# Kernel optimization log

Hardware: AMD Instinct MI355X
Metric: run time of the kernel (lower is better)

The kernel has to match this reference:

```python
import jax, jax.numpy as jnp
import numpy as np

N = 20000      # nodes
E = 256000     # edges
ESM = 1280     # esm_dim
H = 4          # heads
C = 256        # hidden_dim (per-head out)
HC = H * C     # 1024, concat width


def setup_inputs() -> dict:
    key = jax.random.key(0)
    ks = jax.random.split(key, 12)
    s = 0.02
    x = jax.random.normal(ks[0], (N, ESM), jnp.float32)
    edge_index = jax.random.randint(ks[1], (2, E), 0, N, dtype=jnp.int32)
    edge_weights = jax.random.uniform(ks[2], (E,), jnp.float32)
    # GATv2Conv params (PyG): lin_l (src, bias), lin_r (dst, no bias), lin_edge (no bias), att, out bias
    Wl = jax.random.normal(ks[3], (ESM, HC), jnp.float32) * s
    bl = jnp.zeros((HC,), jnp.float32)
    Wr = jax.random.normal(ks[4], (ESM, HC), jnp.float32) * s
    We = jax.random.normal(ks[5], (1, HC), jnp.float32) * s
    att = jax.random.normal(ks[6], (H, C), jnp.float32) * s
    b_gat = jnp.zeros((HC,), jnp.float32)
    # SAGEConv params: lin_l on mean-aggregated neighbors (bias), lin_r on root (no bias)
    Wsl = jax.random.normal(ks[7], (HC, ESM), jnp.float32) * s
    bsl = jnp.zeros((ESM,), jnp.float32)
    Wsr = jax.random.normal(ks[8], (HC, ESM), jnp.float32) * s
    # LayerNorm
    gamma = jnp.ones((ESM,), jnp.float32)
    beta = jnp.zeros((ESM,), jnp.float32)
    return dict(x=x, edge_index=edge_index, edge_weights=edge_weights,
                Wl=Wl, bl=bl, Wr=Wr, We=We, att=att, b_gat=b_gat,
                Wsl=Wsl, bsl=bsl, Wsr=Wsr, gamma=gamma, beta=beta)


def reference(x, edge_index, edge_weights, Wl, bl, Wr, We, att, b_gat,
              Wsl, bsl, Wsr, gamma, beta):
    src, dst = edge_index[0], edge_index[1]
    ew = edge_weights[:, None]                                    # [E,1]
    ones = jnp.ones((E,), x.dtype)
    deg = jax.ops.segment_sum(ones, dst, num_segments=N)          # in-degree [N]
    # ---- GATv2: add self-loops, edge_attr fill_value='mean' (mean of incoming attrs)
    loop_attr = jax.ops.segment_sum(ew, dst, num_segments=N) / jnp.maximum(deg, 1.0)[:, None]
    loop = jnp.arange(N, dtype=src.dtype)
    src_f = jnp.concatenate([src, loop])
    dst_f = jnp.concatenate([dst, loop])
    ea = jnp.concatenate([ew, loop_attr], axis=0)                 # [E+N,1]
    xl = (x @ Wl + bl).reshape(N, H, C)                           # source transform
    xr = (x @ Wr).reshape(N, H, C)                                # target transform
    ee = (ea @ We).reshape(-1, H, C)                              # edge transform
    m = jax.nn.leaky_relu(xl[src_f] + xr[dst_f] + ee, 0.2)        # [E+N,H,C]
    logits = jnp.einsum('ehc,hc->eh', m, att)                     # [E+N,H]
    amax = jax.ops.segment_max(logits, dst_f, num_segments=N)
    ex = jnp.exp(logits - amax[dst_f])
    den = jax.ops.segment_sum(ex, dst_f, num_segments=N)
    alpha = ex / (den[dst_f] + 1e-16)                             # softmax per dst node
    gat = jax.ops.segment_sum(alpha[:, :, None] * xl[src_f], dst_f, num_segments=N)
    gat = gat.reshape(N, HC) + b_gat
    h = jax.nn.elu(gat)
    # ---- SAGEConv: mean neighbor aggregation (no self loops) + root weight
    agg = jax.ops.segment_sum(h[src], dst, num_segments=N) / jnp.maximum(deg, 1.0)[:, None]
    y = jax.nn.relu(agg @ Wsl + bsl + h @ Wsr)
    # ---- residual + LayerNorm
    z = y + x
    mu = jnp.mean(z, axis=-1, keepdims=True)
    var = jnp.mean(jnp.square(z - mu), axis=-1, keepdims=True)
    return (z - mu) * jax.lax.rsqrt(var + 1e-5) * gamma + beta
```

## Files before the change

kernel.cpp:

```cpp
#include <hip/hip_runtime.h>
#include <hip/hip_bf16.h>
#include <math.h>

constexpr int kN   = 20000;
constexpr int kE   = 256000;
constexpr int kESM = 1280;
constexpr int kHC  = 1024;

typedef unsigned int  u32;
typedef unsigned short ushort_t;
typedef __bf16 bf16x8 __attribute__((ext_vector_type(8)));
typedef float  f32x4  __attribute__((ext_vector_type(4)));
typedef unsigned short u16x8 __attribute__((ext_vector_type(8)));
typedef unsigned short u16x4 __attribute__((ext_vector_type(4)));
typedef __attribute__((address_space(1))) const u32 gu32;
typedef __attribute__((address_space(3))) u32 lu32;

static __device__ __forceinline__ unsigned short f2bf_rne(float f) {
    u32 u = __float_as_uint(f);
    u32 r = (u + 0x7FFFu + ((u >> 16) & 1u)) >> 16;
    return (unsigned short)r;
}
static __device__ __forceinline__ float bf2f(unsigned short h) {
    return __uint_as_float(((u32)h) << 16);
}

__global__ __launch_bounds__(256) void deg_kernel(
    const int* __restrict__ dst, const float* __restrict__ ew,
    int* __restrict__ deg, float* __restrict__ wsum)
{
    int e = blockIdx.x * 256 + threadIdx.x;
    if (e < kE) {
        int d = dst[e];
        atomicAdd(&deg[d], 1);
        atomicAdd(&wsum[d], ew[e]);
    }
}

__global__ __launch_bounds__(256) void scan_kernel(
    const int* __restrict__ deg, float* __restrict__ loopat,
    int* __restrict__ offsets)
{
    __shared__ int s[256];
    int tid = threadIdx.x;
    int base = 0;
    if (tid == 0) offsets[0] = 0;
    for (int t0 = 0; t0 < kN; t0 += 256) {
        int i = t0 + tid;
        int d = (i < kN) ? deg[i] : 0;
        if (i < kN) {
            float w = loopat[i];
            loopat[i] = w / fmaxf((float)d, 1.0f);
        }
        s[tid] = d;
        int v = d;
        for (int off = 1; off < 256; off <<= 1) {
            __syncthreads();
            int add = (tid >= off) ? s[tid - off] : 0;
            __syncthreads();
            v += add;
            s[tid] = v;
        }
        __syncthreads();
        if (i < kN) offsets[i + 1] = base + v;
        base += s[255];
        __syncthreads();
    }
}

__global__ __launch_bounds__(256) void sort_kernel(
    const int* __restrict__ src, const int* __restrict__ dst,
    const float* __restrict__ ew, const int* __restrict__ offsets,
    int* __restrict__ cnt, int* __restrict__ ssrc, float* __restrict__ sew)
{
    int e = blockIdx.x * 256 + threadIdx.x;
    if (e < kE) {
        int d = dst[e];
        int p = offsets[d] + atomicAdd(&cnt[d], 1);
        ssrc[p] = src[e];
        sew[p]  = ew[e];
    }
}


__global__ __launch_bounds__(512) void pack_a_kernel(
    const float* __restrict__ A, int M, int K,
    int NKB, ushort_t* __restrict__ dst)
{
    const int kb = blockIdx.x, mb = blockIdx.y;
    const int tid = threadIdx.x;
    const int g = tid >> 7, r = tid & 127;
    const int row = mb * 128 + r;

    u16x8 hi, lo;
    if (row < M) {
        const float* src = A + (size_t)row * K + kb * 32 + g * 8;
        float4 v0 = *(const float4*)src;
        float4 v1 = *(const float4*)(src + 4);
        float vals[8] = {v0.x, v0.y, v0.z, v0.w, v1.x, v1.y, v1.z, v1.w};
#pragma unroll
        for (int j = 0; j < 8; ++j) {
            unsigned short h = f2bf_rne(vals[j]);
            hi[j] = h;
            lo[j] = f2bf_rne(vals[j] - bf2f(h));
        }
    } else {
#pragma unroll
        for (int j = 0; j < 8; ++j) { hi[j] = 0; lo[j] = 0; }
    }
    ushort_t* tb = dst + ((size_t)mb * NKB + kb) * 8192;
    *(u16x8*)&tb[0    + g * 1024 + r * 8] = hi;
    *(u16x8*)&tb[4096 + g * 1024 + r * 8] = lo;
}

__global__ __launch_bounds__(512) void pack_a2_kernel(
    const float* __restrict__ agg, const ushort_t* __restrict__ hb,
    int M, ushort_t* __restrict__ dst)
{
    const int kb = blockIdx.x, mb = blockIdx.y;
    const int tid = threadIdx.x;
    const int g = tid >> 7, r = tid & 127;
    const int row = mb * 128 + r;
    ushort_t* tb = dst + ((size_t)mb * 64 + kb) * 8192;

    if (kb < 32) {
        u16x8 hi, lo;
        if (row < M) {
            const float* src = agg + (size_t)row * 1024 + kb * 32 + g * 8;
            float4 v0 = *(const float4*)src;
            float4 v1 = *(const float4*)(src + 4);
            float vals[8] = {v0.x, v0.y, v0.z, v0.w, v1.x, v1.y, v1.z, v1.w};
#pragma unroll
            for (int j = 0; j < 8; ++j) {
                unsigned short h = f2bf_rne(vals[j]);
                hi[j] = h;
                lo[j] = f2bf_rne(vals[j] - bf2f(h));
            }
        } else {
#pragma unroll
            for (int j = 0; j < 8; ++j) { hi[j] = 0; lo[j] = 0; }
        }
        *(u16x8*)&tb[0    + g * 1024 + r * 8] = hi;
        *(u16x8*)&tb[4096 + g * 1024 + r * 8] = lo;
    } else {
        u16x8 hi;
        if (row < M) {
            hi = *(const u16x8*)&hb[(size_t)row * 1024 + (kb - 32) * 32 + g * 8];
        } else {
#pragma unroll
            for (int j = 0; j < 8; ++j) hi[j] = 0;
        }
        *(u16x8*)&tb[0 + g * 1024 + r * 8] = hi;
    }
}

__global__ __launch_bounds__(512) void pack_b_kernel(
    const float* __restrict__ B1, const float* __restrict__ B2,
    int N, int split, int mode, ushort_t* __restrict__ dst)
{
    const int kb = blockIdx.x, nb = blockIdx.y;
    const int NKB = gridDim.x;
    const int tid = threadIdx.x;
    const int g = tid >> 7, c = tid & 127;
    const int n = nb * 128 + c;

    u16x8 hi, lo;
#pragma unroll
    for (int j = 0; j < 8; ++j) {
        int k = kb * 32 + g * 8 + j;
        float v;
        if (mode == 0) {
            v = (n < split) ? B1[(size_t)k * split + n]
                            : B2[(size_t)k * (N - split) + (n - split)];
        } else {
            v = (k < split) ? B1[(size_t)k * N + n]
                            : B2[(size_t)(k - split) * N + n];
        }
        unsigned short h = f2bf_rne(v);
        hi[j] = h;
        lo[j] = f2bf_rne(v - bf2f(h));
    }
    ushort_t* tb = dst + ((size_t)nb * NKB + kb) * 8192;
    *(u16x8*)&tb[0    + g * 1024 + c * 8] = hi;
    *(u16x8*)&tb[4096 + g * 1024 + c * 8] = lo;
}

__global__ __launch_bounds__(256) void gemm_mfma(
    const ushort_t* __restrict__ Ap, const ushort_t* __restrict__ Bp,
    const float* __restrict__ bias, int biasN,
    const float* __restrict__ resid, float* __restrict__ C,
    int M, int N, int NKB, int nkb_full, int do_relu)
{
    __shared__ ushort_t sb[16384];
    const int tid  = threadIdx.x;
    const int wid  = tid >> 6;
    const int lane = tid & 63;
    const int l15 = lane & 15, l4 = lane >> 4;

    const int nwg = gridDim.x * gridDim.y;
    const int lin = blockIdx.y * gridDim.x + blockIdx.x;
    const int q = nwg >> 3, r = nwg & 7;
    const int xcd = lin & 7, pos = lin >> 3;
    const int swz = (xcd < r ? xcd * (q + 1) : r * (q + 1) + (xcd - r) * q) + pos;
    const int mb = swz / gridDim.x, nb = swz % gridDim.x;
    const int wr = wid >> 1, wc = wid & 1;

    f32x4 acc[4][4];
#pragma unroll
    for (int i = 0; i < 4; ++i)
#pragma unroll
        for (int j = 0; j < 4; ++j) acc[i][j] = (f32x4){0.f, 0.f, 0.f, 0.f};

    const char* at = (const char*)(Ap + (size_t)mb * NKB * 8192);
    const char* bt = (const char*)(Bp + (size_t)nb * NKB * 8192);

    for (int kb = 0; kb < nkb_full; ++kb) {
        const char* atk = at + (size_t)kb * 16384;
        const char* btk = bt + (size_t)kb * 16384;
#pragma unroll
        for (int c = 0; c < 4; ++c) {
            __builtin_amdgcn_global_load_lds(
                (gu32*)(atk + c * 4096 + tid * 16),
                (lu32*)&sb[c * 2048 + wid * 512], 16, 0, 0);
            __builtin_amdgcn_global_load_lds(
                (gu32*)(btk + c * 4096 + tid * 16),
                (lu32*)&sb[8192 + c * 2048 + wid * 512], 16, 0, 0);
        }
        __syncthreads();

        bf16x8 af[2][4], bv[2][4];
#pragma unroll
        for (int hl = 0; hl < 2; ++hl)
#pragma unroll
            for (int m = 0; m < 4; ++m)
                af[hl][m] = *(const bf16x8*)&sb[hl * 4096 + l4 * 1024 + (wr * 64 + m * 16 + l15) * 8];
#pragma unroll
        for (int hl = 0; hl < 2; ++hl)
#pragma unroll
            for (int n = 0; n < 4; ++n)
                bv[hl][n] = *(const bf16x8*)&sb[8192 + hl * 4096 + l4 * 1024 + (wc * 64 + n * 16 + l15) * 8];

#pragma unroll
        for (int m = 0; m < 4; ++m)
#pragma unroll
            for (int n = 0; n < 4; ++n) {
                acc[m][n] = __builtin_amdgcn_mfma_f32_16x16x32_bf16(af[0][m], bv[0][n], acc[m][n], 0, 0, 0);
                acc[m][n] = __builtin_amdgcn_mfma_f32_16x16x32_bf16(af[0][m], bv[1][n], acc[m][n], 0, 0, 0);
                acc[m][n] = __builtin_amdgcn_mfma_f32_16x16x32_bf16(af[1][m], bv[0][n], acc[m][n], 0, 0, 0);
            }
        __syncthreads();
    }

    for (int kb = nkb_full; kb < NKB; ++kb) {
        const char* atk = at + (size_t)kb * 16384;
        const char* btk = bt + (size_t)kb * 16384;
#pragma unroll
        for (int c = 0; c < 2; ++c) {
            __builtin_amdgcn_global_load_lds(
                (gu32*)(atk + c * 4096 + tid * 16),
                (lu32*)&sb[c * 2048 + wid * 512], 16, 0, 0);
        }
#pragma unroll
        for (int c = 0; c < 4; ++c) {
            __builtin_amdgcn_global_load_lds(
                (gu32*)(btk + c * 4096 + tid * 16),
                (lu32*)&sb[8192 + c * 2048 + wid * 512], 16, 0, 0);
        }
        __syncthreads();

        bf16x8 af0[4], bv[2][4];
#pragma unroll
        for (int m = 0; m < 4; ++m)
            af0[m] = *(const bf16x8*)&sb[l4 * 1024 + (wr * 64 + m * 16 + l15) * 8];
#pragma unroll
        for (int hl = 0; hl < 2; ++hl)
#pragma unroll
            for (int n = 0; n < 4; ++n)
                bv[hl][n] = *(const bf16x8*)&sb[8192 + hl * 4096 + l4 * 1024 + (wc * 64 + n * 16 + l15) * 8];

#pragma unroll
        for (int m = 0; m < 4; ++m)
#pragma unroll
            for (int n = 0; n < 4; ++n) {
                acc[m][n] = __builtin_amdgcn_mfma_f32_16x16x32_bf16(af0[m], bv[0][n], acc[m][n], 0, 0, 0);
                acc[m][n] = __builtin_amdgcn_mfma_f32_16x16x32_bf16(af0[m], bv[1][n], acc[m][n], 0, 0, 0);
            }
        __syncthreads();
    }

    const int row_w = mb * 128 + wr * 64;
    const int col_w = nb * 128 + wc * 64;
#pragma unroll
    for (int m = 0; m < 4; ++m) {
#pragma unroll
        for (int n = 0; n < 4; ++n) {
            const int col = col_w + n * 16 + l15;
#pragma unroll
            for (int j = 0; j < 4; ++j) {
                const int row = row_w + m * 16 + l4 * 4 + j;
                if (row < M) {
                    float v = acc[m][n][j];
                    if (bias && col < biasN) v += bias[col];
                    if (do_relu) v = fmaxf(v, 0.f);
                    if (resid) v += resid[(size_t)row * N + col];
                    C[(size_t)row * N + col] = v;
                }
            }
        }
    }
}

__global__ __launch_bounds__(256) void gat2_kernel(
    const float* __restrict__ xlr, const int* __restrict__ ssrc,
    const float* __restrict__ sew, const int* __restrict__ offsets,
    const float* __restrict__ loopat, const float* __restrict__ We,
    const float* __restrict__ att, const float* __restrict__ bgat,
    ushort_t* __restrict__ hout)
{
    const int n = blockIdx.x;
    const int base = threadIdx.x * 4;

    const float4 xr4 = *(const float4*)&xlr[(size_t)n * 2048 + 1024 + base];
    const float4 We4 = *(const float4*)&We[base];
    const float4 at4 = *(const float4*)&att[base];

    float M = -INFINITY, D = 0.f;
    float4 acc = make_float4(0.f, 0.f, 0.f, 0.f);

    const int beg = offsets[n], end = offsets[n + 1];
    for (int e = beg; e <= end; ++e) {
        int s; float w;
        if (e < end) { s = ssrc[e]; w = sew[e]; }
        else         { s = n;       w = loopat[n]; }

        const float4 xls = *(const float4*)&xlr[(size_t)s * 2048 + base];
        float m0 = xls.x + xr4.x + w * We4.x;
        float m1 = xls.y + xr4.y + w * We4.y;
        float m2 = xls.z + xr4.z + w * We4.z;
        float m3 = xls.w + xr4.w + w * We4.w;
        m0 = (m0 >= 0.f) ? m0 : 0.2f * m0;
        m1 = (m1 >= 0.f) ? m1 : 0.2f * m1;
        m2 = (m2 >= 0.f) ? m2 : 0.2f * m2;
        m3 = (m3 >= 0.f) ? m3 : 0.2f * m3;
        float p = m0 * at4.x + m1 * at4.y + m2 * at4.z + m3 * at4.w;
#pragma unroll
        for (int o = 32; o >= 1; o >>= 1) p += __shfl_xor(p, o, 64);

        float newM  = fmaxf(M, p);
        float scale = __expf(M - newM);
        float wexp  = __expf(p - newM);
        D     = D * scale + wexp;
        acc.x = acc.x * scale + wexp * xls.x;
        acc.y = acc.y * scale + wexp * xls.y;
        acc.z = acc.z * scale + wexp * xls.z;
        acc.w = acc.w * scale + wexp * xls.w;
        M = newM;
    }

    const float inv = 1.0f / (D + 1e-16f);
    float g0 = acc.x * inv + bgat[base + 0];
    float g1 = acc.y * inv + bgat[base + 1];
    float g2 = acc.z * inv + bgat[base + 2];
    float g3 = acc.w * inv + bgat[base + 3];
    u16x4 hv;
    hv[0] = f2bf_rne((g0 > 0.f) ? g0 : expm1f(g0));
    hv[1] = f2bf_rne((g1 > 0.f) ? g1 : expm1f(g1));
    hv[2] = f2bf_rne((g2 > 0.f) ? g2 : expm1f(g2));
    hv[3] = f2bf_rne((g3 > 0.f) ? g3 : expm1f(g3));
    *(u16x4*)&hout[(size_t)n * 1024 + base] = hv;
}

__global__ __launch_bounds__(256) void agg2_kernel(
    const ushort_t* __restrict__ hb, const int* __restrict__ ssrc,
    const int* __restrict__ offsets, float* __restrict__ aggout)
{
    const int n = blockIdx.x;
    const int base = threadIdx.x * 4;
    float4 a = make_float4(0.f, 0.f, 0.f, 0.f);
    const int beg = offsets[n], end = offsets[n + 1];
    for (int e = beg; e < end; ++e) {
        const u16x4 hv = *(const u16x4*)&hb[(size_t)ssrc[e] * 1024 + base];
        a.x += bf2f(hv[0]); a.y += bf2f(hv[1]);
        a.z += bf2f(hv[2]); a.w += bf2f(hv[3]);
    }
    const float inv = 1.0f / fmaxf((float)(end - beg), 1.0f);
    a.x *= inv; a.y *= inv; a.z *= inv; a.w *= inv;
    *(float4*)&aggout[(size_t)n * 1024 + base] = a;
}

__global__ __launch_bounds__(320) void ln_kernel(
    float* __restrict__ z, const float* __restrict__ gamma,
    const float* __restrict__ beta)
{
    const int r = blockIdx.x;
    const int t = threadIdx.x;
    const int wave = t >> 6, lane = t & 63;
    __shared__ float red[5];

    float4 v = *(const float4*)&z[(size_t)r * kESM + t * 4];
    float s = v.x + v.y + v.z + v.w;
#pragma unroll
    for (int o = 32; o >= 1; o >>= 1) s += __shfl_xor(s, o, 64);
    if (lane == 0) red[wave] = s;
    __syncthreads();
    s = red[0] + red[1] + red[2] + red[3] + red[4];
    const float mu = s * (1.0f / (float)kESM);

    float dx = v.x - mu, dy = v.y - mu, dz = v.z - mu, dw = v.w - mu;
    float q = dx * dx + dy * dy + dz * dz + dw * dw;
#pragma unroll
    for (int o = 32; o >= 1; o >>= 1) q += __shfl_xor(q, o, 64);
    __syncthreads();
    if (lane == 0) red[wave] = q;
    __syncthreads();
    q = red[0] + red[1] + red[2] + red[3] + red[4];
    const float rstd = rsqrtf(q * (1.0f / (float)kESM) + 1e-5f);

    const float4 g4 = *(const float4*)&gamma[t * 4];
    const float4 b4 = *(const float4*)&beta[t * 4];
    float4 o;
    o.x = dx * rstd * g4.x + b4.x;
    o.y = dy * rstd * g4.y + b4.y;
    o.z = dz * rstd * g4.z + b4.z;
    o.w = dw * rstd * g4.w + b4.w;
    *(float4*)&z[(size_t)r * kESM + t * 4] = o;
}

#define BM 128
#define BN 128
#define BK 16

__global__ __launch_bounds__(256) void gemm_kernel(
    const float* __restrict__ A,  const float* __restrict__ B,
    const float* __restrict__ A2, const float* __restrict__ B2,
    const float* __restrict__ bias, const float* __restrict__ resid,
    float* __restrict__ C, int M, int N, int K, int do_relu)
{
    __shared__ float As[BK][BM];
    __shared__ float Bs[BK][BN];

    const int tid = threadIdx.x;
    const int bm = blockIdx.y, bn = blockIdx.x;
    const int row0 = bm * BM, col0 = bn * BN;
    const int tx = tid & 15, ty = tid >> 4;

    float acc[8][8];
#pragma unroll
    for (int i = 0; i < 8; ++i)
#pragma unroll
        for (int j = 0; j < 8; ++j) acc[i][j] = 0.0f;

    const int arow  = tid >> 1;
    const int akoff = (tid & 1) * 8;
    const int bkr   = tid >> 4;
    const int bcol  = (tid & 15) * 8;

    for (int pair = 0; pair < 2; ++pair) {
        const float* Ap = pair ? A2 : A;
        const float* Bp = pair ? B2 : B;
        if (!Ap) break;
        for (int k0 = 0; k0 < K; k0 += BK) {
            float4 a0 = make_float4(0.f, 0.f, 0.f, 0.f);
            float4 a1 = a0;
            int gr = row0 + arow;
            if (gr < M) {
                const float* aptr = Ap + (size_t)gr * K + k0 + akoff;
                a0 = *(const float4*)aptr;
                a1 = *(const float4*)(aptr + 4);
            }
            const float* bptr = Bp + (size_t)(k0 + bkr) * N + col0 + bcol;
            float4 b0 = *(const float4*)bptr;
            float4 b1 = *(const float4*)(bptr + 4);

            __syncthreads();
            As[akoff + 0][arow] = a0.x;
            As[akoff + 1][arow] = a0.y;
            As[akoff + 2][arow] = a0.z;
            As[akoff + 3][arow] = a0.w;
            As[akoff + 4][arow] = a1.x;
            As[akoff + 5][arow] = a1.y;
            As[akoff + 6][arow] = a1.z;
            As[akoff + 7][arow] = a1.w;
            *(float4*)&Bs[bkr][bcol]     = b0;
            *(float4*)&Bs[bkr][bcol + 4] = b1;
            __syncthreads();

#pragma unroll
            for (int kk = 0; kk < BK; ++kk) {
                float4 a0r = *(const float4*)&As[kk][ty * 8];
                float4 a1r = *(const float4*)&As[kk][ty * 8 + 4];
                float4 b0r = *(const float4*)&Bs[kk][tx * 4];
                float4 b1r = *(const float4*)&Bs[kk][64 + tx * 4];
                float ar[8] = {a0r.x, a0r.y, a0r.z, a0r.w, a1r.x, a1r.y, a1r.z, a1r.w};
                float br[8] = {b0r.x, b0r.y, b0r.z, b0r.w, b1r.x, b1r.y, b1r.z, b1r.w};
#pragma unroll
                for (int i = 0; i < 8; ++i)
#pragma unroll
                    for (int j = 0; j < 8; ++j)
                        acc[i][j] = fmaf(ar[i], br[j], acc[i][j]);
            }
        }
    }

#pragma unroll
    for (int i = 0; i < 8; ++i) {
        int gr = row0 + ty * 8 + i;
        if (gr >= M) break;
#pragma unroll
        for (int half = 0; half < 2; ++half) {
            int gc = col0 + half * 64 + tx * 4;
            float4 out;
            float* o = &out.x;
            const float* rrow = resid ? (resid + (size_t)gr * N + gc) : nullptr;
#pragma unroll
            for (int j = 0; j < 4; ++j) {
                float v = acc[i][half * 4 + j];
                if (bias) v += bias[gc + j];
                if (do_relu) v = fmaxf(v, 0.0f);
                if (rrow) v += rrow[j];
                o[j] = v;
            }
            *(float4*)&C[(size_t)gr * N + gc] = out;
        }
    }
}

__global__ __launch_bounds__(256) void gat_kernel(
    const float* __restrict__ xl, const float* __restrict__ xr,
    const int* __restrict__ ssrc, const float* __restrict__ sew,
    const int* __restrict__ offsets, const float* __restrict__ loopat,
    const float* __restrict__ We, const float* __restrict__ att,
    const float* __restrict__ bgat, float* __restrict__ hout)
{
    const int n = blockIdx.x;
    const int base = threadIdx.x * 4;

    const float4 xr4 = *(const float4*)&xr[(size_t)n * kHC + base];
    const float4 We4 = *(const float4*)&We[base];
    const float4 at4 = *(const float4*)&att[base];

    float M = -INFINITY, D = 0.f;
    float4 acc = make_float4(0.f, 0.f, 0.f, 0.f);

    const int beg = offsets[n], end = offsets[n + 1];
    for (int e = beg; e <= end; ++e) {
        int s; float w;
        if (e < end) { s = ssrc[e]; w = sew[e]; }
        else         { s = n;       w = loopat[n]; }

        const float4 xls = *(const float4*)&xl[(size_t)s * kHC + base];
        float m0 = xls.x + xr4.x + w * We4.x;
        float m1 = xls.y + xr4.y + w * We4.y;
        float m2 = xls.z + xr4.z + w * We4.z;
        float m3 = xls.w + xr4.w + w * We4.w;
        m0 = (m0 >= 0.f) ? m0 : 0.2f * m0;
        m1 = (m1 >= 0.f) ? m1 : 0.2f * m1;
        m2 = (m2 >= 0.f) ? m2 : 0.2f * m2;
        m3 = (m3 >= 0.f) ? m3 : 0.2f * m3;
        float p = m0 * at4.x + m1 * at4.y + m2 * at4.z + m3 * at4.w;
#pragma unroll
        for (int o = 32; o >= 1; o >>= 1) p += __shfl_xor(p, o, 64);

        float newM  = fmaxf(M, p);
        float scale = __expf(M - newM);
        float wexp  = __expf(p - newM);
        D     = D * scale + wexp;
        acc.x = acc.x * scale + wexp * xls.x;
        acc.y = acc.y * scale + wexp * xls.y;
        acc.z = acc.z * scale + wexp * xls.z;
        acc.w = acc.w * scale + wexp * xls.w;
        M = newM;
    }

    const float inv = 1.0f / (D + 1e-16f);
    float g0 = acc.x * inv + bgat[base + 0];
    float g1 = acc.y * inv + bgat[base + 1];
    float g2 = acc.z * inv + bgat[base + 2];
    float g3 = acc.w * inv + bgat[base + 3];
    float4 hv;
    hv.x = (g0 > 0.f) ? g0 : expm1f(g0);
    hv.y = (g1 > 0.f) ? g1 : expm1f(g1);
    hv.z = (g2 > 0.f) ? g2 : expm1f(g2);
    hv.w = (g3 > 0.f) ? g3 : expm1f(g3);
    *(float4*)&hout[(size_t)n * kHC + base] = hv;
}

__global__ __launch_bounds__(256) void agg_kernel(
    const float* __restrict__ h, const int* __restrict__ ssrc,
    const int* __restrict__ offsets, float* __restrict__ aggout)
{
    const int n = blockIdx.x;
    const int base = threadIdx.x * 4;
    float4 a = make_float4(0.f, 0.f, 0.f, 0.f);
    const int beg = offsets[n], end = offsets[n + 1];
    for (int e = beg; e < end; ++e) {
        const float4 hv = *(const float4*)&h[(size_t)ssrc[e] * kHC + base];
        a.x += hv.x; a.y += hv.y; a.z += hv.z; a.w += hv.w;
    }
    const float inv = 1.0f / fmaxf((float)(end - beg), 1.0f);
    a.x *= inv; a.y *= inv; a.z *= inv; a.w *= inv;
    *(float4*)&aggout[(size_t)n * kHC + base] = a;
}

extern "C" void kernel_launch(void* const* d_in, const int* in_sizes, int n_in,
                              void* d_out, int out_size, void* d_ws, size_t ws_size,
                              hipStream_t stream)
{
    const float* x     = (const float*)d_in[0];
    const int*   ei    = (const int*)  d_in[1];
    const float* ew    = (const float*)d_in[2];
    const float* Wl    = (const float*)d_in[3];
    const float* bl    = (const float*)d_in[4];
    const float* Wr    = (const float*)d_in[5];
    const float* We    = (const float*)d_in[6];
    const float* att   = (const float*)d_in[7];
    const float* bgat  = (const float*)d_in[8];
    const float* Wsl   = (const float*)d_in[9];
    const float* bsl   = (const float*)d_in[10];
    const float* Wsr   = (const float*)d_in[11];
    const float* gamma = (const float*)d_in[12];
    const float* beta  = (const float*)d_in[13];
    const int* src = ei;
    const int* dst = ei + kE;
    char* ws = (char*)d_ws;

    const size_t SZ_XPACK = (size_t)157 * 40 * 16384;
    const size_t SZ_XLR   = (size_t)kN * 2048 * 4;
    const size_t SZ_HBUF  = (size_t)kN * 1024 * 2;
    const size_t SZ_B1    = (size_t)16 * 40 * 16384;
    const size_t SZ_B2    = (size_t)10 * 64 * 16384;
    const size_t OFF_XLR  = SZ_XPACK;
    const size_t OFF_HBUF = OFF_XLR + SZ_XLR;
    const size_t OFF_B1   = OFF_HBUF + SZ_HBUF;
    const size_t OFF_B2   = OFF_B1 + SZ_B1;
    size_t off = OFF_B2 + SZ_B2;
    auto salloc = [&](size_t bytes) -> void* {
        void* p = ws + off;
        off = (off + bytes + 255) & ~(size_t)255;
        return p;
    };
    int*   deg    = (int*)  salloc((size_t)kN * 4);
    int*   cnt    = (int*)  salloc((size_t)kN * 4);
    int*   offs   = (int*)  salloc((size_t)(kN + 1) * 4);
    float* loopat = (float*)salloc((size_t)kN * 4);
    int*   ssrc   = (int*)  salloc((size_t)kE * 4);
    float* sew    = (float*)salloc((size_t)kE * 4);
    const size_t FAST_TOTAL = off;

    if (ws_size >= FAST_TOTAL) {
        ushort_t* xpack = (ushort_t*)(ws);
        float*    xlr   = (float*)   (ws + OFF_XLR);
        ushort_t* hbuf  = (ushort_t*)(ws + OFF_HBUF);
        ushort_t* b1p   = (ushort_t*)(ws + OFF_B1);
        ushort_t* b2p   = (ushort_t*)(ws + OFF_B2);
        float*    aggb  = (float*)   (ws + OFF_HBUF - (size_t)kN * 1024 * 4);
        ushort_t* apack = (ushort_t*)(ws);

        hipMemsetAsync(deg,    0, (size_t)kN * 4, stream);
        hipMemsetAsync(cnt,    0, (size_t)kN * 4, stream);
        hipMemsetAsync(loopat, 0, (size_t)kN * 4, stream);

        deg_kernel <<<(kE + 255) / 256, 256, 0, stream>>>(dst, ew, deg, loopat);
        scan_kernel<<<1, 256, 0, stream>>>(deg, loopat, offs);
        sort_kernel<<<(kE + 255) / 256, 256, 0, stream>>>(src, dst, ew, offs, cnt, ssrc, sew);

        pack_a_kernel<<<dim3(40, 157), 512, 0, stream>>>(x, kN, kESM, 40, xpack);
        pack_b_kernel<<<dim3(40, 16), 512, 0, stream>>>(Wl, Wr, 2048, 1024, 0, b1p);
        pack_b_kernel<<<dim3(64, 10), 512, 0, stream>>>(Wsl, Wsr, 1280, 1024, 1, b2p);

        gemm_mfma<<<dim3(16, 157), 256, 0, stream>>>(xpack, b1p, bl, 1024,
                                                     nullptr, xlr, kN, 2048, 40, 40, 0);

        gat2_kernel<<<kN, 256, 0, stream>>>(xlr, ssrc, sew, offs, loopat,
                                            We, att, bgat, hbuf);
        agg2_kernel<<<kN, 256, 0, stream>>>(hbuf, ssrc, offs, aggb);

        pack_a2_kernel<<<dim3(64, 157), 512, 0, stream>>>(aggb, hbuf, kN, apack);

        gemm_mfma<<<dim3(10, 157), 256, 0, stream>>>(apack, b2p, bsl, 1280,
                                                     x, (float*)d_out, kN, 1280, 64, 32, 1);

        ln_kernel<<<kN, 320, 0, stream>>>((float*)d_out, gamma, beta);
    } else {
        size_t foff = 0;
        auto falloc = [&](size_t bytes) -> void* {
            void* p = ws + foff;
            foff = (foff + bytes + 255) & ~(size_t)255;
            return p;
        };
        int*   fdeg    = (int*)  falloc((size_t)kN * 4);
        int*   fcnt    = (int*)  falloc((size_t)kN * 4);
        int*   foffs   = (int*)  falloc((size_t)(kN + 1) * 4);
        float* floopat = (float*)falloc((size_t)kN * 4);
        int*   fssrc   = (int*)  falloc((size_t)kE * 4);
        float* fsew    = (float*)falloc((size_t)kE * 4);
        float* bufA    = (float*)falloc((size_t)kN * kHC * 4);
        float* bufB    = (float*)falloc((size_t)kN * kHC * 4);

        hipMemsetAsync(fdeg,    0, (size_t)kN * 4, stream);
        hipMemsetAsync(fcnt,    0, (size_t)kN * 4, stream);
        hipMemsetAsync(floopat, 0, (size_t)kN * 4, stream);

        deg_kernel <<<(kE + 255) / 256, 256, 0, stream>>>(dst, ew, fdeg, floopat);
        scan_kernel<<<1, 256, 0, stream>>>(fdeg, floopat, foffs);
        sort_kernel<<<(kE + 255) / 256, 256, 0, stream>>>(src, dst, ew, foffs, fcnt, fssrc, fsew);

        dim3 g1(kHC / BN, (kN + BM - 1) / BM);
        gemm_kernel<<<g1, 256, 0, stream>>>(x, Wl, nullptr, nullptr, bl, nullptr,
                                            bufA, kN, kHC, kESM, 0);
        gemm_kernel<<<g1, 256, 0, stream>>>(x, Wr, nullptr, nullptr, nullptr, nullptr,
                                            bufB, kN, kHC, kESM, 0);

        gat_kernel<<<kN, 256, 0, stream>>>(bufA, bufB, fssrc, fsew, foffs, floopat,
                                           We, att, bgat, bufB);
        agg_kernel<<<kN, 256, 0, stream>>>(bufB, fssrc, foffs, bufA);

        dim3 g2(kESM / BN, (kN + BM - 1) / BM);
        gemm_kernel<<<g2, 256, 0, stream>>>(bufA, Wsl, bufB, Wsr, bsl, x,
                                            (float*)d_out, kN, kESM, kHC, 1);

        ln_kernel<<<kN, 320, 0, stream>>>((float*)d_out, gamma, beta);
    }
}
```

Baseline: 1.405 ms.

## Double-buffer LDS in MFMA GEMM to overlap global loads with compute

Doubles the shared-memory tile buffer so the GEMM can prefetch the k-block two steps ahead with global_load_lds while MFMAs run on the current buffer. Manual vmcnt/lgkmcnt waits and raw barriers replace __syncthreads, and the full and tail k-loops are merged into one loop with a predicate. This targets global-load latency that was exposed on every k-step. In exchange LDS use rises to 64KB per block, which may cut occupancy, and the hand-written wait counts must match the number of outstanding loads exactly.

New measurement: 1.494 ms. 1.06x slower.

```diff
diff --git a/kernel.cpp b/kernel.cpp
--- a/kernel.cpp
+++ b/kernel.cpp
@@ -191,7 +191,7 @@
     const float* __restrict__ resid, float* __restrict__ C,
     int M, int N, int NKB, int nkb_full, int do_relu)
 {
-    __shared__ ushort_t sb[16384];
+    __shared__ ushort_t sb[32768];
     const int tid  = threadIdx.x;
     const int wid  = tid >> 6;
     const int lane = tid & 63;
@@ -214,69 +214,55 @@
     const char* at = (const char*)(Ap + (size_t)mb * NKB * 8192);
     const char* bt = (const char*)(Bp + (size_t)nb * NKB * 8192);
 
-    for (int kb = 0; kb < nkb_full; ++kb) {
+    auto stage = [&](int kb, int buf) {
         const char* atk = at + (size_t)kb * 16384;
         const char* btk = bt + (size_t)kb * 16384;
+        const int sbase = buf << 14;
 #pragma unroll
         for (int c = 0; c < 4; ++c) {
             __builtin_amdgcn_global_load_lds(
                 (gu32*)(atk + c * 4096 + tid * 16),
-                (lu32*)&sb[c * 2048 + wid * 512], 16, 0, 0);
+                (lu32*)&sb[sbase + c * 2048 + wid * 512], 16, 0, 0);
             __builtin_amdgcn_global_load_lds(
                 (gu32*)(btk + c * 4096 + tid * 16),
-                (lu32*)&sb[8192 + c * 2048 + wid * 512], 16, 0, 0);
-        }
-        __syncthreads();
-
-        bf16x8 af[2][4], bv[2][4];
+                (lu32*)&sb[sbase + 8192 + c * 2048 + wid * 512], 16, 0, 0);
+        }
+    };
+
+    stage(0, 0);
+    stage(1, 1);
+    asm volatile("s_waitcnt vmcnt(8)" ::: "memory");
+    __builtin_amdgcn_sched_barrier(0);
+    __builtin_amdgcn_s_barrier();
+    __builtin_amdgcn_sched_barrier(0);
+
+    for (int kt = 0; kt < NKB; ++kt) {
+        const int p = kt & 1;
+        const int sbase = p << 14;
+        const bool full = (kt < nkb_full);
+        const bool pre  = (kt + 2 < NKB);
+
+        bf16x8 af0[4], af1[4], bv[2][4];
+#pragma unroll
+        for (int m = 0; m < 4; ++m)
+            af0[m] = *(const bf16x8*)&sb[sbase + l4 * 1024 + (wr * 64 + m * 16 + l15) * 8];
+        if (full) {
+#pragma unroll
+            for (int m = 0; m < 4; ++m)
+                af1[m] = *(const bf16x8*)&sb[sbase + 4096 + l4 * 1024 + (wr * 64 + m * 16 + l15) * 8];
+        }
 #pragma unroll
         for (int hl = 0; hl < 2; ++hl)
 #pragma unroll
-            for (int m = 0; m < 4; ++m)
-                af[hl][m] = *(const bf16x8*)&sb[hl * 4096 + l4 * 1024 + (wr * 64 + m * 16 + l15) * 8];
-#pragma unroll
-        for (int hl = 0; hl < 2; ++hl)
-#pragma unroll
             for (int n = 0; n < 4; ++n)
-                bv[hl][n] = *(const bf16x8*)&sb[8192 + hl * 4096 + l4 * 1024 + (wc * 64 + n * 16 + l15) * 8];
-
-#pragma unroll
-        for (int m = 0; m < 4; ++m)
-#pragma unroll
-            for (int n = 0; n < 4; ++n) {
-                acc[m][n] = __builtin_amdgcn_mfma_f32_16x16x32_bf16(af[0][m], bv[0][n], acc[m][n], 0, 0, 0);
-                acc[m][n] = __builtin_amdgcn_mfma_f32_16x16x32_bf16(af[0][m], bv[1][n], acc[m][n], 0, 0, 0);
-                acc[m][n] = __builtin_amdgcn_mfma_f32_16x16x32_bf16(af[1][m], bv[0][n], acc[m][n], 0, 0, 0);
-            }
-        __syncthreads();
-    }
-
-    for (int kb = nkb_full; kb < NKB; ++kb) {
-        const char* atk = at + (size_t)kb * 16384;
-        const char* btk = bt + (size_t)kb * 16384;
-#pragma unroll
-        for (int c = 0; c < 2; ++c) {
-            __builtin_amdgcn_global_load_lds(
-                (gu32*)(atk + c * 4096 + tid * 16),
-                (lu32*)&sb[c * 2048 + wid * 512], 16, 0, 0);
-        }
-#pragma unroll
-        for (int c = 0; c < 4; ++c) {
-            __builtin_amdgcn_global_load_lds(
-                (gu32*)(btk + c * 4096 + tid * 16),
-                (lu32*)&sb[8192 + c * 2048 + wid * 512], 16, 0, 0);
-        }
-        __syncthreads();
-
-        bf16x8 af0[4], bv[2][4];
-#pragma unroll
-        for (int m = 0; m < 4; ++m)
-            af0[m] = *(const bf16x8*)&sb[l4 * 1024 + (wr * 64 + m * 16 + l15) * 8];
-#pragma unroll
-        for (int hl = 0; hl < 2; ++hl)
-#pragma unroll
-            for (int n = 0; n < 4; ++n)
-                bv[hl][n] = *(const bf16x8*)&sb[8192 + hl * 4096 + l4 * 1024 + (wc * 64 + n * 16 + l15) * 8];
+                bv[hl][n] = *(const bf16x8*)&sb[sbase + 8192 + hl * 4096 + l4 * 1024 + (wc * 64 + n * 16 + l15) * 8];
+
+        asm volatile("s_waitcnt lgkmcnt(0)" ::: "memory");
+        __builtin_amdgcn_sched_barrier(0);
+        __builtin_amdgcn_s_barrier();
+        __builtin_amdgcn_sched_barrier(0);
+
+        if (pre) stage(kt + 2, p);
 
 #pragma unroll
         for (int m = 0; m < 4; ++m)
@@ -285,7 +271,19 @@
                 acc[m][n] = __builtin_amdgcn_mfma_f32_16x16x32_bf16(af0[m], bv[0][n], acc[m][n], 0, 0, 0);
                 acc[m][n] = __builtin_amdgcn_mfma_f32_16x16x32_bf16(af0[m], bv[1][n], acc[m][n], 0, 0, 0);
             }
-        __syncthreads();
+        if (full) {
+#pragma unroll
+            for (int m = 0; m < 4; ++m)
+#pragma unroll
+                for (int n = 0; n < 4; ++n)
+                    acc[m][n] = __builtin_amdgcn_mfma_f32_16x16x32_bf16(af1[m], bv[0][n], acc[m][n], 0, 0, 0);
+        }
+
+        if (pre) { asm volatile("s_waitcnt vmcnt(8)" ::: "memory"); }
+        else     { asm volatile("s_waitcnt vmcnt(0)" ::: "memory"); }
+        __builtin_amdgcn_sched_barrier(0);
+        __builtin_amdgcn_s_barrier();
+        __builtin_amdgcn_sched_barrier(0);
     }
 
     const int row_w = mb * 128 + wr * 64;
```

## Store xl in bf16, compact hi-only A2 blocks, shuffle-based scan

Applied to the files above, without the earlier changes.

The first GEMM epilogue now splits its output: xl (with bias) is written as bf16 to its own buffer and xr stays fp32 in a separate buffer. The GAT kernel then gathers bf16 xl rows per edge, which halves the bytes of the dominant random gather. The bf16-only part of the second GEMM's packed A operand is stored compactly (4096 per block instead of 8192) to shrink pack and load traffic. The single-block scan uses 1024 threads with wave shuffles in place of an LDS Hillis-Steele loop. The risk is lost precision in xl, which now feeds both the attention logits and the aggregation.

Result: faster. 1.282 ms (-8.8%).

```diff
diff --git a/kernel.cpp b/kernel.cpp
--- a/kernel.cpp
+++ b/kernel.cpp
@@ -37,33 +37,39 @@
     }
 }
 
-__global__ __launch_bounds__(256) void scan_kernel(
+__global__ __launch_bounds__(1024) void scan_kernel(
     const int* __restrict__ deg, float* __restrict__ loopat,
     int* __restrict__ offsets)
 {
-    __shared__ int s[256];
-    int tid = threadIdx.x;
+    __shared__ int wsum[16];
+    const int tid = threadIdx.x, wave = tid >> 6, lane = tid & 63;
     int base = 0;
     if (tid == 0) offsets[0] = 0;
-    for (int t0 = 0; t0 < kN; t0 += 256) {
-        int i = t0 + tid;
+    for (int t0 = 0; t0 < kN; t0 += 1024) {
+        const int i = t0 + tid;
         int d = (i < kN) ? deg[i] : 0;
-        if (i < kN) {
-            float w = loopat[i];
-            loopat[i] = w / fmaxf((float)d, 1.0f);
-        }
-        s[tid] = d;
+        if (i < kN) loopat[i] = loopat[i] / fmaxf((float)d, 1.0f);
         int v = d;
-        for (int off = 1; off < 256; off <<= 1) {
-            __syncthreads();
-            int add = (tid >= off) ? s[tid - off] : 0;
-            __syncthreads();
-            v += add;
-            s[tid] = v;
-        }
-        __syncthreads();
-        if (i < kN) offsets[i + 1] = base + v;
-        base += s[255];
+#pragma unroll
+        for (int off = 1; off < 64; off <<= 1) {
+            int u = __shfl_up(v, off, 64);
+            if (lane >= off) v += u;
+        }
+        if (lane == 63) wsum[wave] = v;
+        __syncthreads();
+        if (wave == 0) {
+            int s = (lane < 16) ? wsum[lane] : 0;
+#pragma unroll
+            for (int off = 1; off < 16; off <<= 1) {
+                int u = __shfl_up(s, off, 64);
+                if (lane >= off) s += u;
+            }
+            if (lane < 16) wsum[lane] = s;
+        }
+        __syncthreads();
+        const int prefix = base + (wave ? wsum[wave - 1] : 0);
+        if (i < kN) offsets[i + 1] = prefix + v;
+        base += wsum[15];
         __syncthreads();
     }
 }
@@ -113,6 +119,7 @@
     *(u16x8*)&tb[4096 + g * 1024 + r * 8] = lo;
 }
 
+constexpr size_t kA2Blk = 393216;
 __global__ __launch_bounds__(512) void pack_a2_kernel(
     const float* __restrict__ agg, const ushort_t* __restrict__ hb,
     int M, ushort_t* __restrict__ dst)
@@ -121,9 +128,9 @@
     const int tid = threadIdx.x;
     const int g = tid >> 7, r = tid & 127;
     const int row = mb * 128 + r;
-    ushort_t* tb = dst + ((size_t)mb * 64 + kb) * 8192;
 
     if (kb < 32) {
+        ushort_t* tb = dst + (size_t)mb * kA2Blk + (size_t)kb * 8192;
         u16x8 hi, lo;
         if (row < M) {
             const float* src = agg + (size_t)row * 1024 + kb * 32 + g * 8;
@@ -143,6 +150,7 @@
         *(u16x8*)&tb[0    + g * 1024 + r * 8] = hi;
         *(u16x8*)&tb[4096 + g * 1024 + r * 8] = lo;
     } else {
+        ushort_t* tb = dst + (size_t)mb * kA2Blk + 262144 + (size_t)(kb - 32) * 4096;
         u16x8 hi;
         if (row < M) {
             hi = *(const u16x8*)&hb[(size_t)row * 1024 + (kb - 32) * 32 + g * 8];
@@ -150,7 +158,7 @@
 #pragma unroll
             for (int j = 0; j < 8; ++j) hi[j] = 0;
         }
-        *(u16x8*)&tb[0 + g * 1024 + r * 8] = hi;
+        *(u16x8*)&tb[g * 1024 + r * 8] = hi;
     }
 }
 
@@ -189,6 +197,7 @@
     const ushort_t* __restrict__ Ap, const ushort_t* __restrict__ Bp,
     const float* __restrict__ bias, int biasN,
     const float* __restrict__ resid, float* __restrict__ C,
+    ushort_t* __restrict__ Cbf,
     int M, int N, int NKB, int nkb_full, int do_relu)
 {
     __shared__ ushort_t sb[16384];
@@ -211,7 +220,8 @@
 #pragma unroll
         for (int j = 0; j < 4; ++j) acc[i][j] = (f32x4){0.f, 0.f, 0.f, 0.f};
 
-    const char* at = (const char*)(Ap + (size_t)mb * NKB * 8192);
+    const size_t a_blk = (size_t)nkb_full * 8192 + (size_t)(NKB - nkb_full) * 4096;
+    const char* at = (const char*)(Ap + (size_t)mb * a_blk);
     const char* bt = (const char*)(Bp + (size_t)nb * NKB * 8192);
 
     for (int kb = 0; kb < nkb_full; ++kb) {
@@ -252,7 +262,7 @@
     }
 
     for (int kb = nkb_full; kb < NKB; ++kb) {
-        const char* atk = at + (size_t)kb * 16384;
+        const char* atk = at + (size_t)nkb_full * 16384 + (size_t)(kb - nkb_full) * 8192;
         const char* btk = bt + (size_t)kb * 16384;
 #pragma unroll
         for (int c = 0; c < 2; ++c) {
@@ -290,37 +300,61 @@
 
     const int row_w = mb * 128 + wr * 64;
     const int col_w = nb * 128 + wc * 64;
-#pragma unroll
-    for (int m = 0; m < 4; ++m) {
-#pragma unroll
-        for (int n = 0; n < 4; ++n) {
-            const int col = col_w + n * 16 + l15;
-#pragma unroll
-            for (int j = 0; j < 4; ++j) {
-                const int row = row_w + m * 16 + l4 * 4 + j;
-                if (row < M) {
-                    float v = acc[m][n][j];
-                    if (bias && col < biasN) v += bias[col];
-                    if (do_relu) v = fmaxf(v, 0.f);
-                    if (resid) v += resid[(size_t)row * N + col];
-                    C[(size_t)row * N + col] = v;
+    if (Cbf) {
+        const bool isxl = (col_w < 1024);
+#pragma unroll
+        for (int m = 0; m < 4; ++m) {
+#pragma unroll
+            for (int n = 0; n < 4; ++n) {
+                const int col = col_w + n * 16 + l15;
+#pragma unroll
+                for (int j = 0; j < 4; ++j) {
+                    const int row = row_w + m * 16 + l4 * 4 + j;
+                    if (row < M) {
+                        float v = acc[m][n][j];
+                        if (isxl) {
+                            v += bias[col];
+                            Cbf[(size_t)row * 1024 + col] = f2bf_rne(v);
+                        } else {
+                            C[(size_t)row * 1024 + (col - 1024)] = v;
+                        }
+                    }
                 }
             }
         }
+    } else {
+#pragma unroll
+        for (int m = 0; m < 4; ++m) {
+#pragma unroll
+            for (int n = 0; n < 4; ++n) {
+                const int col = col_w + n * 16 + l15;
+#pragma unroll
+                for (int j = 0; j < 4; ++j) {
+                    const int row = row_w + m * 16 + l4 * 4 + j;
+                    if (row < M) {
+                        float v = acc[m][n][j];
+                        if (bias && col < biasN) v += bias[col];
+                        if (do_relu) v = fmaxf(v, 0.f);
+                        if (resid) v += resid[(size_t)row * N + col];
+                        C[(size_t)row * N + col] = v;
+                    }
+                }
+            }
+        }
     }
 }
 
 __global__ __launch_bounds__(256) void gat2_kernel(
-    const float* __restrict__ xlr, const int* __restrict__ ssrc,
-    const float* __restrict__ sew, const int* __restrict__ offsets,
-    const float* __restrict__ loopat, const float* __restrict__ We,
-    const float* __restrict__ att, const float* __restrict__ bgat,
-    ushort_t* __restrict__ hout)
+    const ushort_t* __restrict__ xlb, const float* __restrict__ xrb,
+    const int* __restrict__ ssrc, const float* __restrict__ sew,
+    const int* __restrict__ offsets, const float* __restrict__ loopat,
+    const float* __restrict__ We, const float* __restrict__ att,
+    const float* __restrict__ bgat, ushort_t* __restrict__ hout)
 {
     const int n = blockIdx.x;
     const int base = threadIdx.x * 4;
 
-    const float4 xr4 = *(const float4*)&xlr[(size_t)n * 2048 + 1024 + base];
+    const float4 xr4 = *(const float4*)&xrb[(size_t)n * 1024 + base];
     const float4 We4 = *(const float4*)&We[base];
     const float4 at4 = *(const float4*)&att[base];
 
@@ -333,7 +367,10 @@
         if (e < end) { s = ssrc[e]; w = sew[e]; }
         else         { s = n;       w = loopat[n]; }
 
-        const float4 xls = *(const float4*)&xlr[(size_t)s * 2048 + base];
+        const u16x4 xh = *(const u16x4*)&xlb[(size_t)s * 1024 + base];
+        float4 xls;
+        xls.x = bf2f(xh[0]); xls.y = bf2f(xh[1]);
+        xls.z = bf2f(xh[2]); xls.w = bf2f(xh[3]);
         float m0 = xls.x + xr4.x + w * We4.x;
         float m1 = xls.y + xr4.y + w * We4.y;
         float m2 = xls.z + xr4.z + w * We4.z;
@@ -600,6 +637,37 @@
     const float inv = 1.0f / fmaxf((float)(end - beg), 1.0f);
     a.x *= inv; a.y *= inv; a.z *= inv; a.w *= inv;
     *(float4*)&aggout[(size_t)n * kHC + base] = a;
+}
+
+__global__ __launch_bounds__(256) void scan_kernel_fb(
+    const int* __restrict__ deg, float* __restrict__ loopat,
+    int* __restrict__ offsets)
+{
+    __shared__ int s[256];
+    int tid = threadIdx.x;
+    int base = 0;
+    if (tid == 0) offsets[0] = 0;
+    for (int t0 = 0; t0 < kN; t0 += 256) {
+        int i = t0 + tid;
+        int d = (i < kN) ? deg[i] : 0;
+        if (i < kN) {
+            float w = loopat[i];
+            loopat[i] = w / fmaxf((float)d, 1.0f);
+        }
+        s[tid] = d;
+        int v = d;
+        for (int off = 1; off < 256; off <<= 1) {
+            __syncthreads();
+            int add = (tid >= off) ? s[tid - off] : 0;
+            __syncthreads();
+            v += add;
+            s[tid] = v;
+        }
+        __syncthreads();
+        if (i < kN) offsets[i + 1] = base + v;
+        base += s[255];
+        __syncthreads();
+    }
 }
 
 extern "C" void kernel_launch(void* const* d_in, const int* in_sizes, int n_in,
@@ -624,15 +692,17 @@
     const int* dst = ei + kE;
     char* ws = (char*)d_ws;
 
-    const size_t SZ_XPACK = (size_t)157 * 40 * 16384;
-    const size_t SZ_XLR   = (size_t)kN * 2048 * 4;
-    const size_t SZ_HBUF  = (size_t)kN * 1024 * 2;
-    const size_t SZ_B1    = (size_t)16 * 40 * 16384;
-    const size_t SZ_B2    = (size_t)10 * 64 * 16384;
-    const size_t OFF_XLR  = SZ_XPACK;
-    const size_t OFF_HBUF = OFF_XLR + SZ_XLR;
-    const size_t OFF_B1   = OFF_HBUF + SZ_HBUF;
-    const size_t OFF_B2   = OFF_B1 + SZ_B1;
+    const size_t SZ_XLB  = (size_t)kN * 1024 * 2;
+    const size_t SZ_XRB  = (size_t)kN * 1024 * 4;
+    const size_t SZ_B1   = (size_t)16 * 40 * 16384;
+    const size_t SZ_XPK  = (size_t)157 * 40 * 16384;
+    const size_t SZ_HBF  = (size_t)kN * 1024 * 2;
+    const size_t SZ_B2   = (size_t)10 * 64 * 16384;
+    const size_t OFF_XRB = SZ_XLB;
+    const size_t OFF_B1  = OFF_XRB + SZ_XRB;
+    const size_t OFF_XPK = OFF_B1 + SZ_B1;
+    const size_t OFF_HBF = OFF_XPK + SZ_XPK;
+    const size_t OFF_B2  = OFF_HBF + SZ_HBF;
     size_t off = OFF_B2 + SZ_B2;
     auto salloc = [&](size_t bytes) -> void* {
         void* p = ws + off;
@@ -648,12 +718,13 @@
     const size_t FAST_TOTAL = off;
 
     if (ws_size >= FAST_TOTAL) {
-        ushort_t* xpack = (ushort_t*)(ws);
-        float*    xlr   = (float*)   (ws + OFF_XLR);
-        ushort_t* hbuf  = (ushort_t*)(ws + OFF_HBUF);
+        ushort_t* xlb   = (ushort_t*)(ws);
+        float*    xrb   = (float*)   (ws + OFF_XRB);
         ushort_t* b1p   = (ushort_t*)(ws + OFF_B1);
+        ushort_t* xpack = (ushort_t*)(ws + OFF_XPK);
+        ushort_t* hbuf  = (ushort_t*)(ws + OFF_HBF);
         ushort_t* b2p   = (ushort_t*)(ws + OFF_B2);
-        float*    aggb  = (float*)   (ws + OFF_HBUF - (size_t)kN * 1024 * 4);
+        float*    aggb  = (float*)   (ws + OFF_XPK);
         ushort_t* apack = (ushort_t*)(ws);
 
         hipMemsetAsync(deg,    0, (size_t)kN * 4, stream);
@@ -661,7 +732,7 @@
         hipMemsetAsync(loopat, 0, (size_t)kN * 4, stream);
 
         deg_kernel <<<(kE + 255) / 256, 256, 0, stream>>>(dst, ew, deg, loopat);
-        scan_kernel<<<1, 256, 0, stream>>>(deg, loopat, offs);
+        scan_kernel<<<1, 1024, 0, stream>>>(deg, loopat, offs);
         sort_kernel<<<(kE + 255) / 256, 256, 0, stream>>>(src, dst, ew, offs, cnt, ssrc, sew);
 
         pack_a_kernel<<<dim3(40, 157), 512, 0, stream>>>(x, kN, kESM, 40, xpack);
@@ -669,16 +740,18 @@
         pack_b_kernel<<<dim3(64, 10), 512, 0, stream>>>(Wsl, Wsr, 1280, 1024, 1, b2p);
 
         gemm_mfma<<<dim3(16, 157), 256, 0, stream>>>(xpack, b1p, bl, 1024,
-                                                     nullptr, xlr, kN, 2048, 40, 40, 0);
-
-        gat2_kernel<<<kN, 256, 0, stream>>>(xlr, ssrc, sew, offs, loopat,
+                                                     nullptr, xrb, xlb,
+                                                     kN, 2048, 40, 40, 0);
+
+        gat2_kernel<<<kN, 256, 0, stream>>>(xlb, xrb, ssrc, sew, offs, loopat,
                                             We, att, bgat, hbuf);
         agg2_kernel<<<kN, 256, 0, stream>>>(hbuf, ssrc, offs, aggb);
 
         pack_a2_kernel<<<dim3(64, 157), 512, 0, stream>>>(aggb, hbuf, kN, apack);
 
         gemm_mfma<<<dim3(10, 157), 256, 0, stream>>>(apack, b2p, bsl, 1280,
-                                                     x, (float*)d_out, kN, 1280, 64, 32, 1);
+                                                     x, (float*)d_out, nullptr,
+                                                     kN, 1280, 64, 32, 1);
 
         ln_kernel<<<kN, 320, 0, stream>>>((float*)d_out, gamma, beta);
     } else {
@@ -702,7 +775,7 @@
         hipMemsetAsync(floopat, 0, (size_t)kN * 4, stream);
 
         deg_kernel <<<(kE + 255) / 256, 256, 0, stream>>>(dst, ew, fdeg, floopat);
-        scan_kernel<<<1, 256, 0, stream>>>(fdeg, floopat, foffs);
+        scan_kernel_fb<<<1, 256, 0, stream>>>(fdeg, floopat, foffs);
         sort_kernel<<<(kE + 255) / 256, 256, 0, stream>>>(src, dst, ew, foffs, fcnt, fssrc, fsew);
 
         dim3 g1(kHC / BN, (kN + BM - 1) / BM);
```
